# Kernel optimization log

Hardware: AMD Instinct MI355X
Metric: run time of the kernel (lower is better)

Reference implementation:

```python
import jax, jax.numpy as jnp
import numpy as np

D_MODEL = 1024
D_STATE = 16
D_CONV = 4
EXPAND = 1
D_INNER = EXPAND * D_MODEL  # must equal D_MODEL for original dt_proj shapes to work
BATCH = 2
SEQ = 2048


def silu(x):
    return x * jax.nn.sigmoid(x)


def setup_inputs() -> dict:
    key = jax.random.key(0)
    ks = jax.random.split(key, 8)
    s = 0.02
    return {
        "x": jax.random.normal(ks[0], (BATCH, SEQ, D_MODEL), dtype=jnp.float32),
        "W_in": jax.random.normal(ks[1], (2 * D_INNER, D_MODEL), dtype=jnp.float32) * s,
        "conv_w": jax.random.normal(ks[2], (D_INNER, D_CONV), dtype=jnp.float32) * s,
        "conv_b": jnp.zeros((D_INNER,), dtype=jnp.float32),
        "W_dt": jax.random.normal(ks[3], (D_INNER, D_INNER), dtype=jnp.float32) * s,
        "b_dt": jnp.zeros((D_INNER,), dtype=jnp.float32),
        "A_log": jnp.zeros((D_INNER, D_STATE), dtype=jnp.float32),  # torch: log(ones)=0
        "Bp": jax.random.normal(ks[4], (D_INNER, D_STATE), dtype=jnp.float32),
        "Cp": jax.random.normal(ks[5], (D_INNER, D_STATE), dtype=jnp.float32),
        "Dp": jnp.ones((D_INNER,), dtype=jnp.float32),
        "W_out": jax.random.normal(ks[6], (D_MODEL, D_INNER), dtype=jnp.float32) * s,
    }


def reference(x, W_in, conv_w, conv_b, W_dt, b_dt, A_log, Bp, Cp, Dp, W_out):
    B, L, _ = x.shape
    # in_proj then split into ssm branch and gating residual
    xr = x @ W_in.T                               # (B, L, 2*D_INNER)
    x_proj, res = jnp.split(xr, 2, axis=-1)       # each (B, L, D_INNER)

    # causal depthwise conv1d (kernel D_CONV), == torch conv1d(padding=K-1)[..., :L]
    xp = jnp.pad(x_proj, ((0, 0), (D_CONV - 1, 0), (0, 0)))
    xc = conv_b + sum(conv_w[:, k] * xp[:, k:k + L, :] for k in range(D_CONV))
    xc = silu(xc)                                 # (B, L, D_INNER)

    # selective SSM scan
    delta = jax.nn.softplus(xc @ W_dt.T + b_dt)   # (B, L, D_INNER)
    A = -jnp.exp(A_log)                           # (D_INNER, D_STATE)
    dA = jnp.exp(delta[..., None] * A)            # (B, L, D_INNER, D_STATE)
    dBx = delta[..., None] * Bp * xc[..., None]   # (B, L, D_INNER, D_STATE)

    def step(h, inp):
        dA_t, dBx_t = inp                         # (B, D_INNER, D_STATE)
        h = dA_t * h + dBx_t
        y = jnp.einsum('bdn,dn->bd', h, Cp)
        return h, y

    h0 = jnp.zeros((B, D_INNER, D_STATE), dtype=x.dtype)
    _, ys = jax.lax.scan(step, h0, (dA.transpose(1, 0, 2, 3), dBx.transpose(1, 0, 2, 3)))
    x_ssm = ys.transpose(1, 0, 2) + xc * Dp       # (B, L, D_INNER)

    return (x_ssm * silu(res)) @ W_out.T          # (B, L, D_MODEL)
```

## Files before the change

kernel.cpp:

```cpp
#include <hip/hip_runtime.h>

typedef unsigned short u16;
typedef __bf16 bf16;
typedef bf16 bf16x8 __attribute__((ext_vector_type(8)));
typedef float f32x4 __attribute__((ext_vector_type(4)));
typedef float f32x16 __attribute__((ext_vector_type(16)));

#define SEQ     2048
#define BATCH   2
#define DM      1024
#define DI      1024
#define NROW    (BATCH*SEQ)
#define NSTATE  16
#define NCHUNK  64
#define CLEN    32

static_assert(SEQ == NCHUNK * CLEN, "chunking must cover SEQ");

__device__ __forceinline__ u16 f2bf(float f) {
  unsigned u = __builtin_bit_cast(unsigned, f);
  u += 0x7FFFu + ((u >> 16) & 1u);
  return (u16)(u >> 16);
}
__device__ __forceinline__ float bf2f(u16 u) {
  return __builtin_bit_cast(float, (unsigned)u << 16);
}
__device__ __forceinline__ float sigm(float x) { return 1.f / (1.f + __expf(-x)); }

__device__ __forceinline__ void gload16(const u16* g, u16* l) {
  __builtin_amdgcn_global_load_lds((const __attribute__((address_space(1))) void*)g,
                                   (__attribute__((address_space(3))) void*)l,
                                   16, 0, 0);
}

__global__ __launch_bounds__(256) void k_cvt_all(
    const float* __restrict__ x, const float* __restrict__ Win,
    const float* __restrict__ Wdt, const float* __restrict__ Wout,
    u16* __restrict__ xbf, u16* __restrict__ winbf,
    u16* __restrict__ wdtbf, u16* __restrict__ woutbf)
{
  long i = (long)blockIdx.x * 256 + threadIdx.x;
  const float* src; u16* dst; long off;
  if (i < 1048576)            { src = x;    dst = xbf;    off = i; }
  else if (i < 1572864)       { src = Win;  dst = winbf;  off = i - 1048576; }
  else if (i < 1835008)       { src = Wdt;  dst = wdtbf;  off = i - 1572864; }
  else                        { src = Wout; dst = woutbf; off = i - 1835008; }
  float4 v = reinterpret_cast<const float4*>(src)[off];
  ushort4 o;
  o.x = f2bf(v.x); o.y = f2bf(v.y); o.z = f2bf(v.z); o.w = f2bf(v.w);
  reinterpret_cast<ushort4*>(dst)[off] = o;
}

__global__ __launch_bounds__(256, 2) void k_gemm1(
    const u16* __restrict__ A, const u16* __restrict__ B,
    u16* __restrict__ outb, u16* __restrict__ outb2, int M, int N, int K)
{
  __shared__ __align__(16) u16 sA[2 * 128 * 64];
  __shared__ __align__(16) u16 sB[2 * 128 * 64];
  const int t = threadIdx.x;
  const int wave = t >> 6, lane = t & 63;
  const int la = lane & 31, hi = lane >> 5;
  const int wr = wave >> 1, wc = wave & 1;

  const int nwg = gridDim.x, bid = blockIdx.x;
  const int wg  = (bid & 7) * (nwg >> 3) + (bid >> 3);
  const long bm = (long)(wg / 16) * 128;
  const long bn = (long)(wg % 16) * 128;

  f32x16 acc[2][2] = {};

  const int srow = t >> 3;
  const int gslot8 = (((t & 7) ^ (srow & 7)) * 8);
  const u16* gA0 = A + (bm + srow) * (long)K + gslot8;
  const u16* gB0 = B + (bn + srow) * (long)K + gslot8;

  auto STAGE = [&](int buf, int k0) {
    #pragma unroll
    for (int i = 0; i < 4; ++i)
      gload16(gA0 + (long)i * 32 * K + k0, &sA[buf * 8192 + i * 2048 + wave * 512]);
    #pragma unroll
    for (int i = 0; i < 4; ++i)
      gload16(gB0 + (long)i * 32 * K + k0, &sB[buf * 8192 + i * 2048 + wave * 512]);
  };

  const int xr = la & 7;
  STAGE(0, 0);
  __syncthreads();
  int cur = 0;
  for (int k0 = 0; k0 < K; k0 += 64) {
    if (k0 + 64 < K) STAGE(cur ^ 1, k0 + 64);
    const u16* pa = &sA[cur * 8192];
    const u16* pb = &sB[cur * 8192];
    bf16x8 af[4][2], bfr[4][2];
    #pragma unroll
    for (int ks = 0; ks < 4; ++ks) {
      const int co = ((ks * 2 + hi) ^ xr) * 8;
      #pragma unroll
      for (int mi = 0; mi < 2; ++mi)
        af[ks][mi] = *reinterpret_cast<const bf16x8*>(pa + (wr * 64 + mi * 32 + la) * 64 + co);
      #pragma unroll
      for (int ni = 0; ni < 2; ++ni)
        bfr[ks][ni] = *reinterpret_cast<const bf16x8*>(pb + (wc * 64 + ni * 32 + la) * 64 + co);
    }
    #pragma unroll
    for (int ks = 0; ks < 4; ++ks)
      #pragma unroll
      for (int mi = 0; mi < 2; ++mi)
        #pragma unroll
        for (int ni = 0; ni < 2; ++ni)
          acc[mi][ni] = __builtin_amdgcn_mfma_f32_32x32x16_bf16(
              af[ks][mi], bfr[ks][ni], acc[mi][ni], 0, 0, 0);
    __syncthreads();
    cur ^= 1;
  }

  #pragma unroll
  for (int mi = 0; mi < 2; ++mi) {
    const long rowb = bm + wr * 64 + mi * 32 + 4 * hi;
    #pragma unroll
    for (int ni = 0; ni < 2; ++ni) {
      const long col = bn + wc * 64 + ni * 32 + la;
      #pragma unroll
      for (int q = 0; q < 4; ++q)
        #pragma unroll
        for (int j = 0; j < 4; ++j) {
          const float v = acc[mi][ni][q * 4 + j];
          const long r = rowb + q * 8 + j;
          if (bn < DI) outb[r * DI + col] = f2bf(v);
          else         outb2[r * DI + (col - DI)] = f2bf(v * sigm(v));
        }
    }
  }
}

template<int EPI>
__global__ __launch_bounds__(512, 1) void k_gemm_skb(
    const u16* __restrict__ A, const u16* __restrict__ B,
    float* __restrict__ outf, u16* __restrict__ outb,
    const float* __restrict__ bias,
    const float* __restrict__ A_log, const float* __restrict__ Bp,
    float* __restrict__ hfin, float* __restrict__ sumdt,
    int M, int N, int K)
{
  __shared__ __align__(16) u16 sStage[32768];
  __shared__ __align__(16) float sX[16384];
  const int t = threadIdx.x;
  const int g  = t >> 8;
  const int tg = t & 255;
  const int wl = (t >> 6) & 3;
  const int lane = t & 63;
  const int lr = lane & 15, kb = lane >> 4;
  const int wr = wl >> 1, wc = wl & 1;

  const int bid = blockIdx.x;
  const int wg  = (bid & 7) * 32 + (bid >> 3);
  const long bm = (long)(wg >> 3) * 128;
  const long bn = (long)(wg & 7) * 128;
  const int kbase = g * (K / 2);

  f32x4 acc[4][4] = {};

  const int srow = tg >> 2;
  const int gslot8 = (((tg & 3) ^ (srow & 3)) * 8);
  const u16* gA0 = A + (bm + srow) * (long)K + gslot8 + kbase;
  const u16* gB0 = B + (bn + srow) * (long)K + gslot8 + kbase;
  u16* lbase = &sStage[g * 16384];
  const int wig = wl * 512;

  auto STAGE = [&](int buf, int k0) {
    gload16(gA0 + k0,                 lbase + buf * 8192 + wig);
    gload16(gA0 + 64 * (long)K + k0,  lbase + buf * 8192 + 2048 + wig);
    gload16(gB0 + k0,                 lbase + buf * 8192 + 4096 + wig);
    gload16(gB0 + 64 * (long)K + k0,  lbase + buf * 8192 + 6144 + wig);
  };

  const int co = ((kb ^ (lr & 3)) * 8);
  STAGE(0, 0);
  __syncthreads();
  int cur = 0;
  const int KS = K / 2;
  for (int k0 = 0; k0 < KS; k0 += 32) {
    if (k0 + 32 < KS) STAGE(cur ^ 1, k0 + 32);
    const u16* pa = lbase + cur * 8192;
    const u16* pb = pa + 4096;
    bf16x8 af[4], bfr[4];
    #pragma unroll
    for (int mi = 0; mi < 4; ++mi)
      af[mi] = *reinterpret_cast<const bf16x8*>(pa + (wr * 64 + mi * 16 + lr) * 32 + co);
    #pragma unroll
    for (int ni = 0; ni < 4; ++ni)
      bfr[ni] = *reinterpret_cast<const bf16x8*>(pb + (wc * 64 + ni * 16 + lr) * 32 + co);
    #pragma unroll
    for (int mi = 0; mi < 4; ++mi)
      #pragma unroll
      for (int ni = 0; ni < 4; ++ni)
        acc[mi][ni] = __builtin_amdgcn_mfma_f32_16x16x32_bf16(
            af[mi], bfr[ni], acc[mi][ni], 0, 0, 0);
    __syncthreads();
    cur ^= 1;
  }

  if (g == 1) {
    #pragma unroll
    for (int mi = 0; mi < 4; ++mi)
      #pragma unroll
      for (int ni = 0; ni < 4; ++ni)
        #pragma unroll
        for (int j = 0; j < 4; ++j)
          sX[(mi * 16 + ni * 4 + j) * 256 + tg] = acc[mi][ni][j];
  }
  __syncthreads();
  if (g == 0) {
    #pragma unroll
    for (int mi = 0; mi < 4; ++mi)
      #pragma unroll
      for (int ni = 0; ni < 4; ++ni)
        #pragma unroll
        for (int j = 0; j < 4; ++j)
          acc[mi][ni][j] += sX[(mi * 16 + ni * 4 + j) * 256 + tg];
  }
  if (EPI == 3) __syncthreads();

  if (g == 0) {
    #pragma unroll
    for (int mi = 0; mi < 4; ++mi) {
      const long row0 = bm + wr * 64 + mi * 16 + kb * 4;
      #pragma unroll
      for (int ni = 0; ni < 4; ++ni) {
        const long col = bn + wc * 64 + ni * 16 + lr;
        #pragma unroll
        for (int j = 0; j < 4; ++j) {
          const float v = acc[mi][ni][j];
          const long r = row0 + j;
          if (EPI == 0) {
            outf[r * N + col] = v;
          } else {
            float z = v + bias[col];
            float sp = fmaxf(z, 0.f) + log1pf(__expf(-fabsf(z)));
            outb[r * N + col] = f2bf(sp);
            sX[(int)(r - bm) * 128 + (int)(col - bn)] = sp;
          }
        }
      }
    }
  }

  if (EPI == 3) {
    __syncthreads();
    const int dl = t & 127;
    const int cl = t >> 7;
    const int d  = (int)bn + dl;
    const int b  = (int)(bm >> 11);
    const int cg = (int)((bm & 2047) >> 5) + cl;
    float Aa[NSTATE], Bb[NSTATE], h[NSTATE];
    #pragma unroll
    for (int n = 0; n < NSTATE; ++n) {
      Aa[n] = -__expf(A_log[d * NSTATE + n]);
      Bb[n] = Bp[d * NSTATE + n];
      h[n] = 0.f;
    }
    float sdt = 0.f;
    const long grow0 = bm + cl * 32;
    for (int i = 0; i < CLEN; ++i) {
      float dt = sX[(cl * 32 + i) * 128 + dl];
      float xv = bf2f(A[(grow0 + i) * (long)K + d]);
      sdt += dt;
      float dx = dt * xv;
      #pragma unroll
      for (int n = 0; n < NSTATE; ++n) {
        float da = __expf(dt * Aa[n]);
        h[n] = fmaf(da, h[n], dx * Bb[n]);
      }
    }
    const long hb = ((long)(b * NCHUNK + cg) * NSTATE) * DI + d;
    #pragma unroll
    for (int n = 0; n < NSTATE; ++n) hfin[hb + (long)n * DI] = h[n];
    sumdt[(long)(b * NCHUNK + cg) * DI + d] = sdt;
  }
}

__global__ __launch_bounds__(256) void k_conv(
    const u16* __restrict__ xproj, const float* __restrict__ convw,
    const float* __restrict__ convb, u16* __restrict__ xcbf)
{
  const int idx = blockIdx.x * 256 + threadIdx.x;
  const int d0 = (idx & 127) * 8;
  const int m  = idx >> 7;
  const int l  = m & (SEQ - 1);
  float acc[8];
  #pragma unroll
  for (int di = 0; di < 8; ++di) acc[di] = convb[d0 + di];
  #pragma unroll
  for (int k = 0; k < 4; ++k) {
    if (l + k - 3 >= 0) {
      ushort4 v2 = *reinterpret_cast<const ushort4*>(&xproj[(long)(m + k - 3) * DI + d0]);
      ushort4 v3 = *reinterpret_cast<const ushort4*>(&xproj[(long)(m + k - 3) * DI + d0 + 4]);
      const u16 vv[8] = {v2.x, v2.y, v2.z, v2.w, v3.x, v3.y, v3.z, v3.w};
      #pragma unroll
      for (int di = 0; di < 8; ++di)
        acc[di] = fmaf(convw[(d0 + di) * 4 + k], bf2f(vv[di]), acc[di]);
    }
  }
  u16 ov[8];
  #pragma unroll
  for (int di = 0; di < 8; ++di) {
    float s = acc[di] * sigm(acc[di]);
    ov[di] = f2bf(s);
  }
  ushort4 o0 = {ov[0], ov[1], ov[2], ov[3]}, o1 = {ov[4], ov[5], ov[6], ov[7]};
  *reinterpret_cast<ushort4*>(&xcbf[(long)m * DI + d0]) = o0;
  *reinterpret_cast<ushort4*>(&xcbf[(long)m * DI + d0 + 4]) = o1;
}

__global__ __launch_bounds__(256) void k_combine(
    const float* __restrict__ hfin, const float* __restrict__ sumdt_buf,
    const float* __restrict__ A_log, float* __restrict__ hstart)
{
  const int idx = blockIdx.x * 256 + threadIdx.x;
  const int d = idx & (DI - 1);
  const int n = (idx >> 10) & (NSTATE - 1);
  const int b = idx >> 14;
  const float Aa = -__expf(A_log[d * NSTATE + n]);
  float h = 0.f;
  for (int c = 0; c < NCHUNK; ++c) {
    const long sb = ((long)(b * NCHUNK + c) * NSTATE + n) * DI + d;
    hstart[sb] = h;
    float sdt = sumdt_buf[(long)(b * NCHUNK + c) * DI + d];
    h = fmaf(__expf(Aa * sdt), h, hfin[sb]);
  }
}

__global__ __launch_bounds__(256) void k_scanB(
    const u16* __restrict__ delta, const u16* __restrict__ xc,
    const float* __restrict__ A_log, const float* __restrict__ Bp,
    const float* __restrict__ Cp, const float* __restrict__ Dp,
    const u16* __restrict__ sres, const float* __restrict__ hstart,
    u16* __restrict__ gated)
{
  const int tid = threadIdx.x, blk = blockIdx.x;
  const int d = (blk & 3) * 256 + tid;
  const int c = (blk >> 2) & (NCHUNK - 1);
  const int b = blk >> 8;
  float Aa[NSTATE], Bb[NSTATE], Cc[NSTATE], h[NSTATE];
  #pragma unroll
  for (int n = 0; n < NSTATE; ++n) {
    Aa[n] = -__expf(A_log[d * NSTATE + n]);
    Bb[n] = Bp[d * NSTATE + n];
    Cc[n] = Cp[d * NSTATE + n];
  }
  const float Dd = Dp[d];
  const long sb = ((long)(b * NCHUNK + c) * NSTATE) * DI + d;
  #pragma unroll
  for (int n = 0; n < NSTATE; ++n) h[n] = hstart[sb + (long)n * DI];
  const long base = ((long)(b * SEQ + c * CLEN)) * DI + d;
  for (int i = 0; i < CLEN; ++i) {
    float dt = bf2f(delta[base + (long)i * DI]);
    float x  = bf2f(xc[base + (long)i * DI]);
    float dx = dt * x;
    float y = 0.f;
    #pragma unroll
    for (int n = 0; n < NSTATE; ++n) {
      float da = __expf(dt * Aa[n]);
      h[n] = fmaf(da, h[n], dx * Bb[n]);
      y = fmaf(h[n], Cc[n], y);
    }
    float xs = fmaf(x, Dd, y);
    float g = xs * bf2f(sres[base + (long)i * DI]);
    gated[base + (long)i * DI] = f2bf(g);
  }
}

extern "C" void kernel_launch(void* const* d_in, const int* in_sizes, int n_in,
                              void* d_out, int out_size, void* d_ws, size_t ws_size,
                              hipStream_t stream)
{
  const float* x      = (const float*)d_in[0];
  const float* W_in   = (const float*)d_in[1];
  const float* conv_w = (const float*)d_in[2];
  const float* conv_b = (const float*)d_in[3];
  const float* W_dt   = (const float*)d_in[4];
  const float* b_dt   = (const float*)d_in[5];
  const float* A_log  = (const float*)d_in[6];
  const float* Bp     = (const float*)d_in[7];
  const float* Cp     = (const float*)d_in[8];
  const float* Dp     = (const float*)d_in[9];
  const float* W_out  = (const float*)d_in[10];
  float* out = (float*)d_out;

  const long MD = (long)NROW * DI;

  char* ws = (char*)d_ws;
  u16*   xproj_bf = (u16*)ws;               ws += MD * 2;
  u16*   silu_bf  = (u16*)ws;               ws += MD * 2;
  u16*   delta_bf = (u16*)ws;               ws += MD * 2;
  u16*   xc_bf    = (u16*)ws;               ws += MD * 2;
  u16*   xbf      = (u16*)ws;               ws += MD * 2;
  u16*   Win_bf   = (u16*)ws;               ws += (long)2 * DI * DM * 2;
  u16*   Wdt_bf   = (u16*)ws;               ws += (long)DI * DI * 2;
  u16*   Wout_bf  = (u16*)ws;               ws += (long)DM * DI * 2;
  float* hfin     = (float*)ws;             ws += (long)BATCH * NCHUNK * NSTATE * DI * 4;
  float* sumdt    = (float*)ws;             ws += (long)BATCH * NCHUNK * DI * 4;
  float* hstart   = (float*)ws;             ws += (long)BATCH * NCHUNK * NSTATE * DI * 4;

  u16* gated = xbf;

  k_cvt_all<<<dim3(8192), dim3(256), 0, stream>>>(
      x, W_in, W_dt, W_out, xbf, Win_bf, Wdt_bf, Wout_bf);

  k_gemm1<<<dim3(512), dim3(256), 0, stream>>>(
      xbf, Win_bf, xproj_bf, silu_bf, NROW, 2 * DI, DM);

  k_conv<<<dim3((unsigned)(MD / 8 / 256)), dim3(256), 0, stream>>>(
      xproj_bf, conv_w, conv_b, xc_bf);

  k_gemm_skb<3><<<dim3(256), dim3(512), 0, stream>>>(
      xc_bf, Wdt_bf, nullptr, delta_bf, b_dt,
      A_log, Bp, hfin, sumdt, NROW, DI, DI);

  k_combine<<<dim3(BATCH * NSTATE * DI / 256), dim3(256), 0, stream>>>(
      hfin, sumdt, A_log, hstart);
  k_scanB<<<dim3(BATCH * NCHUNK * (DI / 256)), dim3(256), 0, stream>>>(
      delta_bf, xc_bf, A_log, Bp, Cp, Dp, silu_bf, hstart, gated);

  k_gemm_skb<0><<<dim3(256), dim3(512), 0, stream>>>(
      gated, Wout_bf, out, nullptr, nullptr,
      nullptr, nullptr, nullptr, nullptr, NROW, DM, DI);
}
```

Measured before the change: 177.2 us.

## Replace split-K GEMM with B-panel-resident GEMM reading A directly from global

```diff
diff --git a/kernel.cpp b/kernel.cpp
--- a/kernel.cpp
+++ b/kernel.cpp
@@ -134,7 +134,7 @@
 }
 
 template<int EPI>
-__global__ __launch_bounds__(512, 1) void k_gemm_skb(
+__global__ __launch_bounds__(512, 1) void k_gemm_bp(
     const u16* __restrict__ A, const u16* __restrict__ B,
     float* __restrict__ outf, u16* __restrict__ outb,
     const float* __restrict__ bias,
@@ -142,104 +142,71 @@
     float* __restrict__ hfin, float* __restrict__ sumdt,
     int M, int N, int K)
 {
-  __shared__ __align__(16) u16 sStage[32768];
-  __shared__ __align__(16) float sX[16384];
+  __shared__ __align__(16) u16 sB[32768];
   const int t = threadIdx.x;
-  const int g  = t >> 8;
-  const int tg = t & 255;
-  const int wl = (t >> 6) & 3;
-  const int lane = t & 63;
+  const int w = t >> 6, lane = t & 63;
   const int lr = lane & 15, kb = lane >> 4;
-  const int wr = wl >> 1, wc = wl & 1;
 
   const int bid = blockIdx.x;
-  const int wg  = (bid & 7) * 32 + (bid >> 3);
-  const long bm = (long)(wg >> 3) * 128;
-  const long bn = (long)(wg & 7) * 128;
-  const int kbase = g * (K / 2);
-
-  f32x4 acc[4][4] = {};
-
-  const int srow = tg >> 2;
-  const int gslot8 = (((tg & 3) ^ (srow & 3)) * 8);
-  const u16* gA0 = A + (bm + srow) * (long)K + gslot8 + kbase;
-  const u16* gB0 = B + (bn + srow) * (long)K + gslot8 + kbase;
-  u16* lbase = &sStage[g * 16384];
-  const int wig = wl * 512;
-
-  auto STAGE = [&](int buf, int k0) {
-    gload16(gA0 + k0,                 lbase + buf * 8192 + wig);
-    gload16(gA0 + 64 * (long)K + k0,  lbase + buf * 8192 + 2048 + wig);
-    gload16(gB0 + k0,                 lbase + buf * 8192 + 4096 + wig);
-    gload16(gB0 + 64 * (long)K + k0,  lbase + buf * 8192 + 6144 + wig);
-  };
-
-  const int co = ((kb ^ (lr & 3)) * 8);
-  STAGE(0, 0);
+  const int wg  = (bid & 7) * 64 + (bid >> 3);
+  const int ns  = wg >> 4;
+  const long n0 = (long)ns * 32;
+  const long bm = (long)(wg & 15) * 256;
+
+  #pragma unroll
+  for (int i = 0; i < 8; ++i) {
+    const int G = i * 512 + t;
+    const int col = G >> 7;
+    const int gp  = G & 127;
+    const int gg  = gp ^ (col & 7);
+    gload16(B + (n0 + col) * (long)K + gg * 8,
+            &sB[i * 4096 + w * 512 + (lane) * 8]);
+  }
   __syncthreads();
-  int cur = 0;
-  const int KS = K / 2;
-  for (int k0 = 0; k0 < KS; k0 += 32) {
-    if (k0 + 32 < KS) STAGE(cur ^ 1, k0 + 32);
-    const u16* pa = lbase + cur * 8192;
-    const u16* pb = pa + 4096;
-    bf16x8 af[4], bfr[4];
-    #pragma unroll
-    for (int mi = 0; mi < 4; ++mi)
-      af[mi] = *reinterpret_cast<const bf16x8*>(pa + (wr * 64 + mi * 16 + lr) * 32 + co);
-    #pragma unroll
-    for (int ni = 0; ni < 4; ++ni)
-      bfr[ni] = *reinterpret_cast<const bf16x8*>(pb + (wc * 64 + ni * 16 + lr) * 32 + co);
-    #pragma unroll
-    for (int mi = 0; mi < 4; ++mi)
-      #pragma unroll
-      for (int ni = 0; ni < 4; ++ni)
-        acc[mi][ni] = __builtin_amdgcn_mfma_f32_16x16x32_bf16(
-            af[mi], bfr[ni], acc[mi][ni], 0, 0, 0);
-    __syncthreads();
-    cur ^= 1;
-  }
-
-  if (g == 1) {
-    #pragma unroll
-    for (int mi = 0; mi < 4; ++mi)
-      #pragma unroll
-      for (int ni = 0; ni < 4; ++ni)
-        #pragma unroll
-        for (int j = 0; j < 4; ++j)
-          sX[(mi * 16 + ni * 4 + j) * 256 + tg] = acc[mi][ni][j];
-  }
-  __syncthreads();
-  if (g == 0) {
-    #pragma unroll
-    for (int mi = 0; mi < 4; ++mi)
-      #pragma unroll
-      for (int ni = 0; ni < 4; ++ni)
-        #pragma unroll
-        for (int j = 0; j < 4; ++j)
-          acc[mi][ni][j] += sX[(mi * 16 + ni * 4 + j) * 256 + tg];
-  }
+
+  f32x4 acc[2][2] = {};
+  const long row0 = bm + w * 32;
+  const u16* a0 = A + (row0 + lr) * (long)K + kb * 8;
+  const u16* a1 = A + (row0 + 16 + lr) * (long)K + kb * 8;
+  const int bswz = lr & 7;
+
+  #pragma unroll 4
+  for (int k0 = 0; k0 < K; k0 += 32) {
+    bf16x8 af0 = *reinterpret_cast<const bf16x8*>(a0 + k0);
+    bf16x8 af1 = *reinterpret_cast<const bf16x8*>(a1 + k0);
+    const int g  = (k0 >> 3) + kb;
+    const int bo = ((g ^ bswz) * 8);
+    bf16x8 bfr[2];
+    #pragma unroll
+    for (int nf = 0; nf < 2; ++nf)
+      bfr[nf] = *reinterpret_cast<const bf16x8*>(&sB[(nf * 16 + lr) * 1024 + bo]);
+    #pragma unroll
+    for (int nf = 0; nf < 2; ++nf) {
+      acc[0][nf] = __builtin_amdgcn_mfma_f32_16x16x32_bf16(af0, bfr[nf], acc[0][nf], 0, 0, 0);
+      acc[1][nf] = __builtin_amdgcn_mfma_f32_16x16x32_bf16(af1, bfr[nf], acc[1][nf], 0, 0, 0);
+    }
+  }
+
+  float* sD = (float*)sB;
   if (EPI == 3) __syncthreads();
 
-  if (g == 0) {
-    #pragma unroll
-    for (int mi = 0; mi < 4; ++mi) {
-      const long row0 = bm + wr * 64 + mi * 16 + kb * 4;
-      #pragma unroll
-      for (int ni = 0; ni < 4; ++ni) {
-        const long col = bn + wc * 64 + ni * 16 + lr;
-        #pragma unroll
-        for (int j = 0; j < 4; ++j) {
-          const float v = acc[mi][ni][j];
-          const long r = row0 + j;
-          if (EPI == 0) {
-            outf[r * N + col] = v;
-          } else {
-            float z = v + bias[col];
-            float sp = fmaxf(z, 0.f) + log1pf(__expf(-fabsf(z)));
-            outb[r * N + col] = f2bf(sp);
-            sX[(int)(r - bm) * 128 + (int)(col - bn)] = sp;
-          }
+  #pragma unroll
+  for (int mi = 0; mi < 2; ++mi) {
+    const long r0 = row0 + mi * 16 + kb * 4;
+    #pragma unroll
+    for (int nf = 0; nf < 2; ++nf) {
+      const long col = n0 + nf * 16 + lr;
+      #pragma unroll
+      for (int j = 0; j < 4; ++j) {
+        const float v = acc[mi][nf][j];
+        const long r = r0 + j;
+        if (EPI == 0) {
+          outf[r * N + col] = v;
+        } else {
+          float z = v + bias[col];
+          float sp = fmaxf(z, 0.f) + log1pf(__expf(-fabsf(z)));
+          outb[r * N + col] = f2bf(sp);
+          sD[(int)(r - bm) * 32 + (int)(col - n0)] = sp;
         }
       }
     }
@@ -247,35 +214,36 @@
 
   if (EPI == 3) {
     __syncthreads();
-    const int dl = t & 127;
-    const int cl = t >> 7;
-    const int d  = (int)bn + dl;
+    const int pair = t >> 1, half = t & 1;
+    const int cl = pair >> 5;
+    const int dl = pair & 31;
+    const int d  = (int)n0 + dl;
     const int b  = (int)(bm >> 11);
     const int cg = (int)((bm & 2047) >> 5) + cl;
-    float Aa[NSTATE], Bb[NSTATE], h[NSTATE];
-    #pragma unroll
-    for (int n = 0; n < NSTATE; ++n) {
-      Aa[n] = -__expf(A_log[d * NSTATE + n]);
-      Bb[n] = Bp[d * NSTATE + n];
+    float Aa[8], Bb[8], h[8];
+    #pragma unroll
+    for (int n = 0; n < 8; ++n) {
+      Aa[n] = -__expf(A_log[d * NSTATE + half * 8 + n]);
+      Bb[n] = Bp[d * NSTATE + half * 8 + n];
       h[n] = 0.f;
     }
     float sdt = 0.f;
     const long grow0 = bm + cl * 32;
     for (int i = 0; i < CLEN; ++i) {
-      float dt = sX[(cl * 32 + i) * 128 + dl];
+      float dt = sD[(cl * 32 + i) * 32 + dl];
       float xv = bf2f(A[(grow0 + i) * (long)K + d]);
       sdt += dt;
       float dx = dt * xv;
       #pragma unroll
-      for (int n = 0; n < NSTATE; ++n) {
+      for (int n = 0; n < 8; ++n) {
         float da = __expf(dt * Aa[n]);
         h[n] = fmaf(da, h[n], dx * Bb[n]);
       }
     }
-    const long hb = ((long)(b * NCHUNK + cg) * NSTATE) * DI + d;
-    #pragma unroll
-    for (int n = 0; n < NSTATE; ++n) hfin[hb + (long)n * DI] = h[n];
-    sumdt[(long)(b * NCHUNK + cg) * DI + d] = sdt;
+    const long hb = ((long)(b * NCHUNK + cg) * NSTATE + half * 8) * DI + d;
+    #pragma unroll
+    for (int n = 0; n < 8; ++n) hfin[hb + (long)n * DI] = h[n];
+    if (half == 0) sumdt[(long)(b * NCHUNK + cg) * DI + d] = sdt;
   }
 }
 
@@ -413,7 +381,7 @@
   k_conv<<<dim3((unsigned)(MD / 8 / 256)), dim3(256), 0, stream>>>(
       xproj_bf, conv_w, conv_b, xc_bf);
 
-  k_gemm_skb<3><<<dim3(256), dim3(512), 0, stream>>>(
+  k_gemm_bp<3><<<dim3(512), dim3(512), 0, stream>>>(
       xc_bf, Wdt_bf, nullptr, delta_bf, b_dt,
       A_log, Bp, hfin, sumdt, NROW, DI, DI);
 
@@ -422,7 +390,7 @@
   k_scanB<<<dim3(BATCH * NCHUNK * (DI / 256)), dim3(256), 0, stream>>>(
       delta_bf, xc_bf, A_log, Bp, Cp, Dp, silu_bf, hstart, gated);
 
-  k_gemm_skb<0><<<dim3(256), dim3(512), 0, stream>>>(
+  k_gemm_bp<0><<<dim3(512), dim3(512), 0, stream>>>(
       gated, Wout_bf, out, nullptr, nullptr,
       nullptr, nullptr, nullptr, nullptr, NROW, DM, DI);
 }
```

New measurement: 194.7 us. +9.9%, slower.
